# Kernel tuning notes

Measured on AMD Instinct MI355X. Metric: run time of the kernel, lower is better.

## Reference

```python
import jax, jax.numpy as jnp
import numpy as np

INPUT_DIM = 512
HIDDEN_DIM = 1024
NUM_LAYERS = 2
B, S = 32, 512


def _xavier(key, shape):
    fan_out, fan_in = shape
    limit = float(np.sqrt(6.0 / (fan_in + fan_out)))
    return jax.random.uniform(key, shape, jnp.float32, -limit, limit)


def setup_inputs() -> dict:
    key = jax.random.key(0)
    ks = jax.random.split(key, 8)
    x = jax.random.normal(ks[0], (B, S, INPUT_DIM), jnp.float32)
    # layer 0: input_dim -> hidden, layer 1: hidden -> hidden
    Wih0 = _xavier(ks[1], (3 * HIDDEN_DIM, INPUT_DIM))
    Whh0 = _xavier(ks[2], (3 * HIDDEN_DIM, HIDDEN_DIM))
    b0 = jnp.zeros((3 * HIDDEN_DIM,), jnp.float32)
    Wih1 = _xavier(ks[3], (3 * HIDDEN_DIM, HIDDEN_DIM))
    Whh1 = _xavier(ks[4], (3 * HIDDEN_DIM, HIDDEN_DIM))
    b1 = jnp.zeros((3 * HIDDEN_DIM,), jnp.float32)
    Wlin = _xavier(ks[5], (INPUT_DIM, HIDDEN_DIM))
    blin = jnp.zeros((INPUT_DIM,), jnp.float32)
    return {"x": x, "Wih0": Wih0, "Whh0": Whh0, "b0": b0,
            "Wih1": Wih1, "Whh1": Whh1, "b1": b1,
            "Wlin": Wlin, "blin": blin}


def _gru_layer(x_tm, h0, Wih, Whh, b):
    # x_tm: [S, B, D_in] time-major; h0: [B, H]
    H = HIDDEN_DIM
    Whn = Whh[2 * H: 3 * H]  # [H, H] used twice per the original cell

    def step(h, x_t):
        gates = x_t @ Wih.T + h @ Whh.T + b          # [B, 3H]
        r, z, n = jnp.split(gates, 3, axis=1)
        r = jax.nn.sigmoid(r)
        z = jax.nn.sigmoid(z)
        # NOTE: original cell adds h@Whn a second time, scaled by r (nonstandard)
        n = jnp.tanh(n + r * (h @ Whn.T))
        h_new = (1.0 - z) * n + z * h
        return h_new, h_new

    h_last, ys = jax.lax.scan(step, h0, x_tm)
    return ys, h_last  # ys: [S, B, H]


def reference(x, Wih0, Whh0, b0, Wih1, Whh1, b1, Wlin, blin):
    # dropout=0.0 -> identity (eval mode)
    x_tm = jnp.swapaxes(x, 0, 1)  # [S, B, D]
    h0 = jnp.zeros((x.shape[0], HIDDEN_DIM), x.dtype)
    y0, h_last0 = _gru_layer(x_tm, h0, Wih0, Whh0, b0)
    y1, h_last1 = _gru_layer(y0, h0, Wih1, Whh1, b1)
    layer_output = jnp.swapaxes(y1, 0, 1)            # [B, S, H]
    out = layer_output @ Wlin.T + blin               # [B, S, INPUT_DIM]
    new_hidden = jnp.stack([h_last0, h_last1], axis=0)  # [L, B, H]
    return out, new_hidden
```

## Files before the change

### kernel.cpp

```cpp
#include <hip/hip_runtime.h>
#include <math.h>

#define B_  32
#define S_  512
#define H_  1024
#define G3_ 3072
#define SENT32 0x7F7F7F7Fu

typedef __attribute__((ext_vector_type(8))) short bf16x8;
typedef __attribute__((ext_vector_type(4))) float f32x4;
typedef __attribute__((ext_vector_type(4))) unsigned int u32x4;

__device__ __forceinline__ unsigned short f2bf(float f) {
  unsigned int u = __float_as_uint(f);
  u = (u + 0x7FFFu + ((u >> 16) & 1u)) >> 16;
  return (unsigned short)u;
}

__device__ __forceinline__ void ld4_mall(const unsigned short* p, u32x4& r) {
  asm volatile("global_load_dwordx4 %0, %1, off sc0 sc1" : "=v"(r) : "v"(p));
}
__device__ __forceinline__ void st_mall_b32(unsigned short* p, unsigned int v) {
  asm volatile("global_store_dword %0, %1, off sc0 sc1" :: "v"(p), "v"(v) : "memory");
}

#define BAR_LGKM() do {                                   \
  __builtin_amdgcn_sched_barrier(0);                      \
  asm volatile("s_waitcnt lgkmcnt(0)" ::: "memory");      \
  __builtin_amdgcn_s_barrier();                           \
  __builtin_amdgcn_sched_barrier(0);                      \
} while (0)

__global__ void cast_f32_bf16(const float* __restrict__ in, unsigned short* __restrict__ out, int n) {
  int i = blockIdx.x * 256 + threadIdx.x;
  if (i < n) out[i] = f2bf(in[i]);
}

__global__ void cast_transpose_x(const float* __restrict__ x, unsigned short* __restrict__ xtm) {
  int s = blockIdx.x & 511, b = blockIdx.x >> 9;
  int k = threadIdx.x * 4;
  float4 v = *(const float4*)(x + ((size_t)b * S_ + s) * 512 + k);
  ushort4 o = { f2bf(v.x), f2bf(v.y), f2bf(v.z), f2bf(v.w) };
  *(ushort4*)(xtm + ((size_t)s * B_ + b) * 512 + k) = o;
}

template<int APERM, int CPERM, typename CT>
__global__ __launch_bounds__(256)
void gemm_bf16(const unsigned short* __restrict__ A, const unsigned short* __restrict__ W,
               const float* __restrict__ bias, CT* __restrict__ C, int M, int N, int K) {
  __shared__ __align__(16) unsigned short As[128 * 40];
  __shared__ __align__(16) unsigned short Ws[128 * 40];
  const int tid   = threadIdx.x;
  const int mBase = blockIdx.y * 128;
  const int nBase = blockIdx.x * 128;
  const int lane  = tid & 63;
  const int w     = tid >> 6;
  const int wm    = (w & 1) * 64;
  const int wn    = (w >> 1) * 64;
  const int r16   = lane & 15;
  const int q     = lane >> 4;

  f32x4 acc[4][4];
  for (int i = 0; i < 4; ++i)
    for (int j = 0; j < 4; ++j)
      for (int t = 0; t < 4; ++t) acc[i][j][t] = 0.f;

  const int r0  = tid >> 2;
  const int kk0 = (tid & 3) * 8;

  for (int k0 = 0; k0 < K; k0 += 32) {
    {
      int r = r0;
      size_t ar = APERM ? ((size_t)((mBase + r) & 31) * S_ + (size_t)((mBase + r) >> 5)) : (size_t)(mBase + r);
      *(uint4*)&As[r * 40 + kk0] = *(const uint4*)(A + ar * K + k0 + kk0);
      int r2 = r + 64;
      size_t ar2 = APERM ? ((size_t)((mBase + r2) & 31) * S_ + (size_t)((mBase + r2) >> 5)) : (size_t)(mBase + r2);
      *(uint4*)&As[r2 * 40 + kk0] = *(const uint4*)(A + ar2 * K + k0 + kk0);
      *(uint4*)&Ws[r * 40 + kk0]  = *(const uint4*)(W + (size_t)(nBase + r)  * K + k0 + kk0);
      *(uint4*)&Ws[r2 * 40 + kk0] = *(const uint4*)(W + (size_t)(nBase + r2) * K + k0 + kk0);
    }
    __syncthreads();
    bf16x8 af[4], bfr[4];
#pragma unroll
    for (int i = 0; i < 4; ++i) af[i]  = *(const bf16x8*)&As[(wm + i * 16 + r16) * 40 + q * 8];
#pragma unroll
    for (int j = 0; j < 4; ++j) bfr[j] = *(const bf16x8*)&Ws[(wn + j * 16 + r16) * 40 + q * 8];
#pragma unroll
    for (int i = 0; i < 4; ++i)
#pragma unroll
      for (int j = 0; j < 4; ++j)
        acc[i][j] = __builtin_amdgcn_mfma_f32_16x16x32_bf16(af[i], bfr[j], acc[i][j], 0, 0, 0);
    __syncthreads();
  }

#pragma unroll
  for (int i = 0; i < 4; ++i)
#pragma unroll
    for (int j = 0; j < 4; ++j)
#pragma unroll
      for (int t = 0; t < 4; ++t) {
        int m = mBase + wm + i * 16 + q * 4 + t;
        int n = nBase + wn + j * 16 + r16;
        float v = acc[i][j][t] + bias[n];
        size_t crow = CPERM ? ((size_t)(m & 31) * S_ + (size_t)(m >> 5)) : (size_t)m;
        if constexpr (sizeof(CT) == 4) C[crow * N + n] = v;
        else                           C[crow * N + n] = f2bf(v);
      }
}


__global__ __launch_bounds__(512, 2)
void gru_fused(const unsigned short* __restrict__ wih0, const unsigned short* __restrict__ whh0,
               const float* __restrict__ b0,
               const unsigned short* __restrict__ wih1, const unsigned short* __restrict__ whh1,
               const float* __restrict__ b1,
               const unsigned short* __restrict__ xtm, const unsigned short* __restrict__ zerosB,
               unsigned short* __restrict__ hx0, unsigned short* __restrict__ hx1,
               unsigned short* __restrict__ y1,
               float* __restrict__ hlast0, float* __restrict__ hlast1) {
  __shared__ __align__(16) float part[8 * 2 * 3 * 64 * 4];
  const int tid  = threadIdx.x;
  const int lane = tid & 63;
  const int w    = tid >> 6;
  const int r16  = lane & 15;
  const int q    = lane >> 4;
  const bool L1  = blockIdx.x >= 64;
  const int  j0  = (L1 ? (int)blockIdx.x - 64 : (int)blockIdx.x) * 16;
  const int  myblk = j0 >> 4;
  const bool hiw = w >= 4;

  const unsigned short* Wsrc;
  int wstride, kbase, ncha;
  if (!L1) {
    if (!hiw) { Wsrc = wih0; wstride = 512;  kbase = w * 128;       ncha = 4; }
    else      { Wsrc = whh0; wstride = 1024; kbase = (w - 4) * 256; ncha = 8; }
  } else {
    if (!hiw) { Wsrc = wih1; wstride = 1024; kbase = w * 256;       ncha = 8; }
    else      { Wsrc = whh1; wstride = 1024; kbase = (w - 4) * 256; ncha = 8; }
  }
  const int blkbase = kbase >> 4;

  bf16x8 bw[3][8];
#pragma unroll
  for (int g = 0; g < 3; ++g)
#pragma unroll
    for (int c = 0; c < 8; ++c)
      if (c < ncha)
        bw[g][c] = *(const bf16x8*)(Wsrc + (size_t)(g * H_ + j0 + r16) * wstride + kbase + c * 32 + q * 8);

  const int eb  = tid >> 4;
  const int ejj = tid & 15;
  const int em  = eb >> 4, eq2 = (eb >> 2) & 3, ereg = eb & 3;
  const float* bias = L1 ? b1 : b0;
  const float brv = bias[j0 + ejj];
  const float bzv = bias[H_ + j0 + ejj];
  const float bnv = bias[2 * H_ + j0 + ejj];
  float phv = 0.f;

  unsigned short* hxbuf = L1 ? hx1 : hx0;
  float*          hlast = L1 ? hlast1 : hlast0;

  const int hxLaneOff = ((q >> 1) * 512) + r16 * 16 + (q & 1) * 8;

  for (int t = 0; t < S_; ++t) {
    union AU { unsigned int dd[4]; u32x4 u4; bf16x8 v; };
    AU a0[8], a1[8];
    bool plain;
    const unsigned short* pp = nullptr;
    int pstride = 0;
    const unsigned short* hp = nullptr;
    if (!hiw) {
      if (!L1) { plain = true;  pp = xtm + (size_t)t * B_ * 512; pstride = 512; }
      else     { plain = false; hp = hx0 + ((size_t)t * 64 + blkbase) * 512 + hxLaneOff; }
    } else {
      if (t == 0) { plain = true;  pp = zerosB; pstride = 1024; }
      else        { plain = false; hp = hxbuf + ((size_t)(t - 1) * 64 + blkbase) * 512 + hxLaneOff; }
    }
    if (plain) {
      const unsigned short* ap0 = pp + (size_t)r16 * pstride + kbase + q * 8;
      const unsigned short* ap1 = ap0 + 16 * pstride;
#pragma unroll
      for (int c = 0; c < 8; ++c) if (c < ncha) {
        a0[c].v = *(const bf16x8*)(ap0 + c * 32);
        a1[c].v = *(const bf16x8*)(ap1 + c * 32);
      }
    } else {
      int spins = 0;
      for (;;) {
#pragma unroll
        for (int c = 0; c < 8; ++c) {
          ld4_mall(hp + c * 1024, a0[c].u4);
          ld4_mall(hp + c * 1024 + 256, a1[c].u4);
        }
        asm volatile("s_waitcnt vmcnt(0)"
          : "+v"(a0[0].u4), "+v"(a0[1].u4), "+v"(a0[2].u4), "+v"(a0[3].u4),
            "+v"(a0[4].u4), "+v"(a0[5].u4), "+v"(a0[6].u4), "+v"(a0[7].u4),
            "+v"(a1[0].u4), "+v"(a1[1].u4), "+v"(a1[2].u4), "+v"(a1[3].u4),
            "+v"(a1[4].u4), "+v"(a1[5].u4), "+v"(a1[6].u4), "+v"(a1[7].u4)
          :: "memory");
        __builtin_amdgcn_sched_barrier(0);
        int ok = 1;
#pragma unroll
        for (int c = 0; c < 8; ++c)
#pragma unroll
          for (int d = 0; d < 4; ++d)
            ok &= (a0[c].dd[d] != SENT32) & (a1[c].dd[d] != SENT32);
        if (__all(ok)) break;
        if (++spins > (1 << 20)) break;
        if (spins > 8) __builtin_amdgcn_s_sleep(1);
      }
    }

    f32x4 acc[2][3];
#pragma unroll
    for (int m = 0; m < 2; ++m)
#pragma unroll
      for (int g = 0; g < 3; ++g)
#pragma unroll
        for (int u = 0; u < 4; ++u) acc[m][g][u] = 0.f;

#pragma unroll
    for (int c = 0; c < 8; ++c) if (c < ncha)
#pragma unroll
      for (int g = 0; g < 3; ++g) {
        acc[0][g] = __builtin_amdgcn_mfma_f32_16x16x32_bf16(a0[c].v, bw[g][c], acc[0][g], 0, 0, 0);
        acc[1][g] = __builtin_amdgcn_mfma_f32_16x16x32_bf16(a1[c].v, bw[g][c], acc[1][g], 0, 0, 0);
      }

#pragma unroll
    for (int m = 0; m < 2; ++m)
#pragma unroll
      for (int g = 0; g < 3; ++g)
        *(f32x4*)&part[(((w * 2 + m) * 3 + g) * 64 + lane) * 4] = acc[m][g];
    BAR_LGKM();

    {
      float hr = 0.f, hz = 0.f, nx = 0.f, nh = 0.f;
#pragma unroll
      for (int ww = 0; ww < 8; ++ww) {
        int base = (ww * 2 + em) * 3;
        float vr = part[((base + 0) * 64 + eq2 * 16 + ejj) * 4 + ereg];
        float vz = part[((base + 1) * 64 + eq2 * 16 + ejj) * 4 + ereg];
        float vn = part[((base + 2) * 64 + eq2 * 16 + ejj) * 4 + ereg];
        hr += vr; hz += vz;
        if (ww < 4) nx += vn; else nh += vn;
      }
      float r  = __builtin_amdgcn_rcpf(1.f + __expf(-(hr + brv)));
      float z  = __builtin_amdgcn_rcpf(1.f + __expf(-(hz + bzv)));
      float a2 = nx + bnv + nh + r * nh;
      float nn = 1.f - 2.f * __builtin_amdgcn_rcpf(__expf(2.f * a2) + 1.f);
      float hv = (1.f - z) * nn + z * phv;
      phv = hv;
      float other = __shfl_xor(hv, 1);
      if ((ejj & 1) == 0) {
        unsigned int pk = (unsigned int)f2bf(hv) | ((unsigned int)f2bf(other) << 16);
        st_mall_b32(hxbuf + ((size_t)t * 64 + myblk) * 512 + eb * 16 + ejj, pk);
        if (L1)
          *(unsigned int*)(y1 + ((size_t)t * B_ + eb) * H_ + j0 + ejj) = pk;
        if (t == S_ - 1) {
          hlast[eb * H_ + j0 + ejj]     = hv;
          hlast[eb * H_ + j0 + ejj + 1] = other;
        }
      }
    }
    BAR_LGKM();
  }
}

extern "C" void kernel_launch(void* const* d_in, const int* in_sizes, int n_in,
                              void* d_out, int out_size, void* d_ws, size_t ws_size,
                              hipStream_t stream) {
  const float* x    = (const float*)d_in[0];
  const float* Wih0 = (const float*)d_in[1];
  const float* Whh0 = (const float*)d_in[2];
  const float* b0   = (const float*)d_in[3];
  const float* Wih1 = (const float*)d_in[4];
  const float* Whh1 = (const float*)d_in[5];
  const float* b1   = (const float*)d_in[6];
  const float* Wlin = (const float*)d_in[7];
  const float* blin = (const float*)d_in[8];
  float* out = (float*)d_out;

  char* p = (char*)d_ws;
  size_t off = 0;
  auto alloc = [&](size_t bytes) { void* r = p + off; off += (bytes + 255) & ~(size_t)255; return r; };

  unsigned short* xtm   = (unsigned short*)alloc((size_t)8388608 * 2);
  unsigned short* wih0b = (unsigned short*)alloc((size_t)1572864 * 2);
  unsigned short* whh0b = (unsigned short*)alloc((size_t)3145728 * 2);
  unsigned short* wih1b = (unsigned short*)alloc((size_t)3145728 * 2);
  unsigned short* whh1b = (unsigned short*)alloc((size_t)3145728 * 2);
  unsigned short* wlinb = (unsigned short*)alloc((size_t)524288 * 2);
  unsigned short* hx0   = (unsigned short*)alloc((size_t)16777216 * 2);
  unsigned short* hx1   = (unsigned short*)alloc((size_t)16777216 * 2);
  unsigned short* y1b   = (unsigned short*)alloc((size_t)16777216 * 2);
  unsigned short* zerosB= (unsigned short*)alloc((size_t)B_ * H_ * 2);

  (void)hipMemsetAsync(hx0, 0x7F, (size_t)16777216 * 2, stream);
  (void)hipMemsetAsync(hx1, 0x7F, (size_t)16777216 * 2, stream);
  (void)hipMemsetAsync(zerosB, 0, (size_t)B_ * H_ * 2, stream);

  auto cast = [&](const float* in, unsigned short* o, int n) {
    cast_f32_bf16<<<n / 256, 256, 0, stream>>>(in, o, n);
  };
  cast_transpose_x<<<16384, 128, 0, stream>>>(x, xtm);
  cast(Wih0, wih0b, 1572864);
  cast(Whh0, whh0b, 3145728);
  cast(Wih1, wih1b, 3145728);
  cast(Whh1, whh1b, 3145728);
  cast(Wlin, wlinb, 524288);

  float* hlast0 = out + 8388608;
  float* hlast1 = out + 8388608 + B_ * H_;

  gru_fused<<<128, 512, 0, stream>>>(wih0b, whh0b, b0, wih1b, whh1b, b1,
                                     xtm, zerosB, hx0, hx1, y1b, hlast0, hlast1);

  {
    dim3 g(512 / 128, 16384 / 128);
    gemm_bf16<0, 1, float><<<g, 256, 0, stream>>>(y1b, wlinb, blin, out, 16384, 512, 1024);
  }
}
```

Baseline: 1.893 ms.

## Fuse output linear projection into persistent GRU kernel as consumer blocks

Adds 32 extra persistent blocks to the fused GRU kernel. Each one spins on the layer-1 hidden-state buffer for every timestep and computes the output linear projection with MFMA, writing fp32 results directly. This removes the separate GEMM launch and the y1 bf16 staging buffer, so the projection overlaps with the recurrence. In exchange it adds polling traffic on hx1 and relies on all 160 blocks being co-resident. The projection also becomes a sequence of small per-timestep tiles rather than one large GEMM.

```diff
diff --git a/kernel.cpp b/kernel.cpp
--- a/kernel.cpp
+++ b/kernel.cpp
@@ -42,70 +42,6 @@
   float4 v = *(const float4*)(x + ((size_t)b * S_ + s) * 512 + k);
   ushort4 o = { f2bf(v.x), f2bf(v.y), f2bf(v.z), f2bf(v.w) };
   *(ushort4*)(xtm + ((size_t)s * B_ + b) * 512 + k) = o;
-}
-
-template<int APERM, int CPERM, typename CT>
-__global__ __launch_bounds__(256)
-void gemm_bf16(const unsigned short* __restrict__ A, const unsigned short* __restrict__ W,
-               const float* __restrict__ bias, CT* __restrict__ C, int M, int N, int K) {
-  __shared__ __align__(16) unsigned short As[128 * 40];
-  __shared__ __align__(16) unsigned short Ws[128 * 40];
-  const int tid   = threadIdx.x;
-  const int mBase = blockIdx.y * 128;
-  const int nBase = blockIdx.x * 128;
-  const int lane  = tid & 63;
-  const int w     = tid >> 6;
-  const int wm    = (w & 1) * 64;
-  const int wn    = (w >> 1) * 64;
-  const int r16   = lane & 15;
-  const int q     = lane >> 4;
-
-  f32x4 acc[4][4];
-  for (int i = 0; i < 4; ++i)
-    for (int j = 0; j < 4; ++j)
-      for (int t = 0; t < 4; ++t) acc[i][j][t] = 0.f;
-
-  const int r0  = tid >> 2;
-  const int kk0 = (tid & 3) * 8;
-
-  for (int k0 = 0; k0 < K; k0 += 32) {
-    {
-      int r = r0;
-      size_t ar = APERM ? ((size_t)((mBase + r) & 31) * S_ + (size_t)((mBase + r) >> 5)) : (size_t)(mBase + r);
-      *(uint4*)&As[r * 40 + kk0] = *(const uint4*)(A + ar * K + k0 + kk0);
-      int r2 = r + 64;
-      size_t ar2 = APERM ? ((size_t)((mBase + r2) & 31) * S_ + (size_t)((mBase + r2) >> 5)) : (size_t)(mBase + r2);
-      *(uint4*)&As[r2 * 40 + kk0] = *(const uint4*)(A + ar2 * K + k0 + kk0);
-      *(uint4*)&Ws[r * 40 + kk0]  = *(const uint4*)(W + (size_t)(nBase + r)  * K + k0 + kk0);
-      *(uint4*)&Ws[r2 * 40 + kk0] = *(const uint4*)(W + (size_t)(nBase + r2) * K + k0 + kk0);
-    }
-    __syncthreads();
-    bf16x8 af[4], bfr[4];
-#pragma unroll
-    for (int i = 0; i < 4; ++i) af[i]  = *(const bf16x8*)&As[(wm + i * 16 + r16) * 40 + q * 8];
-#pragma unroll
-    for (int j = 0; j < 4; ++j) bfr[j] = *(const bf16x8*)&Ws[(wn + j * 16 + r16) * 40 + q * 8];
-#pragma unroll
-    for (int i = 0; i < 4; ++i)
-#pragma unroll
-      for (int j = 0; j < 4; ++j)
-        acc[i][j] = __builtin_amdgcn_mfma_f32_16x16x32_bf16(af[i], bfr[j], acc[i][j], 0, 0, 0);
-    __syncthreads();
-  }
-
-#pragma unroll
-  for (int i = 0; i < 4; ++i)
-#pragma unroll
-    for (int j = 0; j < 4; ++j)
-#pragma unroll
-      for (int t = 0; t < 4; ++t) {
-        int m = mBase + wm + i * 16 + q * 4 + t;
-        int n = nBase + wn + j * 16 + r16;
-        float v = acc[i][j][t] + bias[n];
-        size_t crow = CPERM ? ((size_t)(m & 31) * S_ + (size_t)(m >> 5)) : (size_t)m;
-        if constexpr (sizeof(CT) == 4) C[crow * N + n] = v;
-        else                           C[crow * N + n] = f2bf(v);
-      }
 }
 
 
@@ -116,7 +52,8 @@
                const float* __restrict__ b1,
                const unsigned short* __restrict__ xtm, const unsigned short* __restrict__ zerosB,
                unsigned short* __restrict__ hx0, unsigned short* __restrict__ hx1,
-               unsigned short* __restrict__ y1,
+               const unsigned short* __restrict__ wlin, const float* __restrict__ blin,
+               float* __restrict__ out,
                float* __restrict__ hlast0, float* __restrict__ hlast1) {
   __shared__ __align__(16) float part[8 * 2 * 3 * 64 * 4];
   const int tid  = threadIdx.x;
@@ -124,6 +61,74 @@
   const int w    = tid >> 6;
   const int r16  = lane & 15;
   const int q    = lane >> 4;
+
+  union AU { unsigned int dd[4]; u32x4 u4; bf16x8 v; };
+
+  if (blockIdx.x >= 128) {
+    const int nj0 = ((int)blockIdx.x - 128) * 16;
+    const int kbase = w * 128;
+    const int blkbase = kbase >> 4;
+    bf16x8 bwp[4];
+#pragma unroll
+    for (int c = 0; c < 4; ++c)
+      bwp[c] = *(const bf16x8*)(wlin + (size_t)(nj0 + r16) * H_ + kbase + c * 32 + q * 8);
+    const int eb = tid >> 4, ejj = tid & 15;
+    const int em = eb >> 4, eq2 = (eb >> 2) & 3, ereg = eb & 3;
+    const float bl = blin[nj0 + ejj];
+    const int hxLaneOff = ((q >> 1) * 512) + r16 * 16 + (q & 1) * 8;
+
+    for (int t = 0; t < S_; ++t) {
+      const unsigned short* hp = hx1 + ((size_t)t * 64 + blkbase) * 512 + hxLaneOff;
+      AU a0[4], a1[4];
+      int spins = 0;
+      for (;;) {
+#pragma unroll
+        for (int c = 0; c < 4; ++c) {
+          ld4_mall(hp + c * 1024, a0[c].u4);
+          ld4_mall(hp + c * 1024 + 256, a1[c].u4);
+        }
+        asm volatile("s_waitcnt vmcnt(0)"
+          : "+v"(a0[0].u4), "+v"(a0[1].u4), "+v"(a0[2].u4), "+v"(a0[3].u4),
+            "+v"(a1[0].u4), "+v"(a1[1].u4), "+v"(a1[2].u4), "+v"(a1[3].u4)
+          :: "memory");
+        __builtin_amdgcn_sched_barrier(0);
+        int ok = 1;
+#pragma unroll
+        for (int c = 0; c < 4; ++c)
+#pragma unroll
+          for (int d = 0; d < 4; ++d)
+            ok &= (a0[c].dd[d] != SENT32) & (a1[c].dd[d] != SENT32);
+        if (__all(ok)) break;
+        if (++spins > (1 << 21)) break;
+        if (spins > 8) __builtin_amdgcn_s_sleep(1);
+      }
+
+      f32x4 acc[2];
+#pragma unroll
+      for (int m = 0; m < 2; ++m)
+#pragma unroll
+        for (int u = 0; u < 4; ++u) acc[m][u] = 0.f;
+#pragma unroll
+      for (int c = 0; c < 4; ++c) {
+        acc[0] = __builtin_amdgcn_mfma_f32_16x16x32_bf16(a0[c].v, bwp[c], acc[0], 0, 0, 0);
+        acc[1] = __builtin_amdgcn_mfma_f32_16x16x32_bf16(a1[c].v, bwp[c], acc[1], 0, 0, 0);
+      }
+#pragma unroll
+      for (int m = 0; m < 2; ++m)
+        *(f32x4*)&part[((w * 2 + m) * 64 + lane) * 4] = acc[m];
+      BAR_LGKM();
+      {
+        float s = 0.f;
+#pragma unroll
+        for (int ww = 0; ww < 8; ++ww)
+          s += part[((ww * 2 + em) * 64 + eq2 * 16 + ejj) * 4 + ereg];
+        out[((size_t)eb * S_ + t) * 512 + nj0 + ejj] = s + bl;
+      }
+      BAR_LGKM();
+    }
+    return;
+  }
+
   const bool L1  = blockIdx.x >= 64;
   const int  j0  = (L1 ? (int)blockIdx.x - 64 : (int)blockIdx.x) * 16;
   const int  myblk = j0 >> 4;
@@ -163,7 +168,6 @@
   const int hxLaneOff = ((q >> 1) * 512) + r16 * 16 + (q & 1) * 8;
 
   for (int t = 0; t < S_; ++t) {
-    union AU { unsigned int dd[4]; u32x4 u4; bf16x8 v; };
     AU a0[8], a1[8];
     bool plain;
     const unsigned short* pp = nullptr;
@@ -255,8 +259,6 @@
       if ((ejj & 1) == 0) {
         unsigned int pk = (unsigned int)f2bf(hv) | ((unsigned int)f2bf(other) << 16);
         st_mall_b32(hxbuf + ((size_t)t * 64 + myblk) * 512 + eb * 16 + ejj, pk);
-        if (L1)
-          *(unsigned int*)(y1 + ((size_t)t * B_ + eb) * H_ + j0 + ejj) = pk;
         if (t == S_ - 1) {
           hlast[eb * H_ + j0 + ejj]     = hv;
           hlast[eb * H_ + j0 + ejj + 1] = other;
@@ -293,7 +295,6 @@
   unsigned short* wlinb = (unsigned short*)alloc((size_t)524288 * 2);
   unsigned short* hx0   = (unsigned short*)alloc((size_t)16777216 * 2);
   unsigned short* hx1   = (unsigned short*)alloc((size_t)16777216 * 2);
-  unsigned short* y1b   = (unsigned short*)alloc((size_t)16777216 * 2);
   unsigned short* zerosB= (unsigned short*)alloc((size_t)B_ * H_ * 2);
 
   (void)hipMemsetAsync(hx0, 0x7F, (size_t)16777216 * 2, stream);
@@ -313,11 +314,7 @@
   float* hlast0 = out + 8388608;
   float* hlast1 = out + 8388608 + B_ * H_;
 
-  gru_fused<<<128, 512, 0, stream>>>(wih0b, whh0b, b0, wih1b, whh1b, b1,
-                                     xtm, zerosB, hx0, hx1, y1b, hlast0, hlast1);
-
-  {
-    dim3 g(512 / 128, 16384 / 128);
-    gemm_bf16<0, 1, float><<<g, 256, 0, stream>>>(y1b, wlinb, blin, out, 16384, 512, 1024);
-  }
-}
+  gru_fused<<<160, 512, 0, stream>>>(wih0b, whh0b, b0, wih1b, whh1b, b1,
+                                     xtm, zerosB, hx0, hx1, wlinb, blin, out,
+                                     hlast0, hlast1);
+}
```

Result: slower. 1.942 ms (+2.6%).
